# Performance work log

Hardware: AMD Instinct MI355X
Metric: run time of the kernel (lower is better)

Reference implementation:

```python
import jax, jax.numpy as jnp
import numpy as np

BL = 512  # block length (matches init bl)


def _conv1x1(w, b, x):
    # w: (out, in), b: (out,), x: (batch, in, L) -> (batch, out, L)
    return jnp.einsum('oi,bil->bol', w, x) + b[None, :, None]


def _window_mask(bl):
    # Faithful to torch loop: window_mask[:, :, i:i+bl] = 1 for i in range(bl)
    # -> all ones except the last column.
    wm = np.zeros((1, bl, bl + 2 * (bl // 2)), np.float32)
    for i in range(bl):
        wm[:, :, i:i + bl] = 1.0
    return jnp.asarray(wm)


def setup_inputs() -> dict:
    key = jax.random.key(0)
    ks = jax.random.split(key, 5)
    B, C, L = 1, 2048, 16384
    Cq = C // 2  # r1 = r2 = r3 = 2
    s_in = 1.0 / float(np.sqrt(C))
    s_mid = 1.0 / float(np.sqrt(Cq))
    return {
        'x1': jax.random.normal(ks[0], (B, C, L), jnp.float32),
        'x2': jnp.zeros((B, C, L), jnp.float32),
        'mask': jnp.ones((B, 1, L), jnp.float32),
        'wq': jax.random.normal(ks[1], (Cq, C), jnp.float32) * s_in,
        'bq': jnp.zeros((Cq,), jnp.float32),
        'wk': jax.random.normal(ks[2], (Cq, C), jnp.float32) * s_in,
        'bk': jnp.zeros((Cq,), jnp.float32),
        'wv': jax.random.normal(ks[3], (Cq, C), jnp.float32) * s_in,
        'bv': jnp.zeros((Cq,), jnp.float32),
        'wo': jax.random.normal(ks[4], (C, Cq), jnp.float32) * s_mid,
        'bo': jnp.zeros((C,), jnp.float32),
    }


def reference(x1, x2, mask, wq, bq, wk, bk, wv, bv, wo, bo):
    B, C, L = x1.shape  # B == 1 (asserted by sliding path)
    bl = BL
    nb = L // bl  # L % bl == 0 by construction
    half = bl // 2

    q = _conv1x1(wq, bq, x1)  # (1, c, L)
    k = _conv1x1(wk, bk, x1)
    v = _conv1x1(wv, bv, x1)  # encoder stage: value from x1 (x2 unused)
    c = q.shape[1]

    # query blocks: (nb, c, bl)
    qb = q.reshape(B, c, nb, bl).transpose(0, 2, 1, 3).reshape(nb, c, bl)

    # pad k/v/padding_mask with bl//2 zeros on both sides, then take overlapping
    # windows of width 2*bl per block.
    kp = jnp.pad(k, ((0, 0), (0, 0), (half, half)))[0]            # (c, L+bl)
    vp = jnp.pad(v, ((0, 0), (0, 0), (half, half)))[0]
    pm = jnp.pad(mask[:, 0:1, :], ((0, 0), (0, 0), (half, half)))[0]  # (1, L+bl)
    cols = np.arange(nb)[:, None] * bl + np.arange(2 * bl)[None, :]   # (nb, 2bl)
    kb = kp[:, cols].transpose(1, 0, 2)   # (nb, c, 2bl)
    vb = vp[:, cols].transpose(1, 0, 2)   # (nb, c, 2bl)
    pmb = pm[:, cols].transpose(1, 0, 2)  # (nb, 1, 2bl)

    final_mask = _window_mask(bl) * pmb   # (nb, bl, 2bl)

    # scalar dot attention with log-mask (as in AttentionHelper.scalar_dot_att)
    energy = jnp.einsum('ncl,ncm->nlm', qb, kb) / jnp.float32(np.sqrt(c))
    attn = jax.nn.softmax(energy + jnp.log(final_mask + 1e-9), axis=-1)
    attn = attn * final_mask
    out = jnp.einsum('ncm,nlm->ncl', vb, attn)  # (nb, c, bl)

    out = _conv1x1(wo, bo, jax.nn.relu(out))    # (nb, C, bl)
    out = out.reshape(B, nb, C, bl).transpose(0, 2, 1, 3).reshape(B, C, nb * bl)
    out = out[:, :, :L]
    return out * mask[:, 0:1, :]
```

## Files before the change

### kernel.cpp

```cpp
#include <hip/hip_runtime.h>
#include <hip/hip_bf16.h>

typedef __attribute__((ext_vector_type(4))) float f32x4;
typedef __attribute__((ext_vector_type(8))) __bf16 bf16x8;

#define DEVINL static __device__ __forceinline__

DEVINL unsigned short f2bf(float f) {
  union { float f; unsigned u; } x; x.f = f;
  return (unsigned short)((x.u + 0x7FFFu + ((x.u >> 16) & 1u)) >> 16);
}

DEVINL void gload16(const void* g, void* l) {
  __builtin_amdgcn_global_load_lds((const __attribute__((address_space(1))) void*)g,
                                   (__attribute__((address_space(3))) void*)l,
                                   16, 0, 0);
}

#define SBAR()  asm volatile("s_barrier" ::: "memory")
#define LGKM0() asm volatile("s_waitcnt lgkmcnt(0)" ::: "memory")
#define VM(n)   asm volatile("s_waitcnt vmcnt(" #n ")" ::: "memory")

__global__ __launch_bounds__(256) void transpose_x_k(const float* __restrict__ x,
                                                     unsigned short* __restrict__ xT) {
  __shared__ float tile[32][33];
  const int bx = blockIdx.x;
  const int by = blockIdx.y;
  const int tx = threadIdx.x;
  const int ty = threadIdx.y;
#pragma unroll
  for (int i = 0; i < 4; ++i) {
    int c = by * 32 + ty + i * 8;
    tile[ty + i * 8][tx] = x[(long)c * 16384 + bx * 32 + tx];
  }
  __syncthreads();
#pragma unroll
  for (int i = 0; i < 4; ++i) {
    int l = bx * 32 + ty + i * 8;
    xT[(long)l * 2048 + by * 32 + tx] = f2bf(tile[tx][ty + i * 8]);
  }
}

__global__ __launch_bounds__(256) void conv_w_k(const float* __restrict__ wq,
                                                const float* __restrict__ wk,
                                                const float* __restrict__ wv,
                                                const float* __restrict__ wo,
                                                unsigned short* __restrict__ Wqk,
                                                unsigned short* __restrict__ Wv,
                                                unsigned short* __restrict__ Wo) {
  long i = (long)blockIdx.x * 256 + threadIdx.x;
  if (i < 4194304) {
    float s = (i < 2097152) ? wq[i] : wk[i - 2097152];
    Wqk[i] = f2bf(s);
  } else if (i < 6291456) {
    Wv[i - 4194304] = f2bf(wv[i - 4194304]);
  } else {
    Wo[i - 6291456] = f2bf(wo[i - 6291456]);
  }
}

enum { EPI_QK = 0, EPI_V = 1, EPI_S = 2, EPI_PV = 3, EPI_OUT = 4 };

struct GArgs {
  const unsigned short* A;
  const unsigned short* Bt;
  void* C;
  const float* bias;
  const float* bias2;
  const float* mask;
  const unsigned short* guard;
  int aBatch, cBatch;
  int btRow0, btRow0Step, btRowLim;
  int btK0, btK0Step, btKLim;
};

template <int EPI, int LDA, int LDB, int LDC, int KK>
__global__ __launch_bounds__(512, 2) void gemm8_k(GArgs g) {
  constexpr int NK = KK >> 6;
  constexpr int NT = NK >> 1;
  __shared__ char lds[131072];

  const int t = threadIdx.x;
  const int l = t & 63;
  const int w = t >> 6;
  const int Nbase = blockIdx.x << 8;
  const int Mbase = blockIdx.y << 8;
  const int z = blockIdx.z;

  const int wr = w >> 2;
  const int wc = w & 3;
  const int fr = l & 15;
  const int fg = l >> 4;

  const unsigned short* Ab = g.A + (long)z * g.aBatch + (long)Mbase * LDA;
  const int bRowBase = g.btRow0 + z * g.btRow0Step + Nbase;
  const int bK0 = g.btK0 + z * g.btK0Step;

  const int rr = t >> 3;
  const int cb8s = t & 7;

  auto stage = [&](int bufSel, int unit, int kt) {
    const int k0 = (kt & (NK - 1)) << 6;
    const bool isA = (unit == 0) || (unit == 3);
#pragma unroll
    for (int gph = 0; gph < 2; ++gph) {
      int row;
      if (isA) row = (unit == 0 ? 0 : 64) + (gph << 7) + rr;
      else     row = (unit == 1 ? 0 : 32) + (gph << 7) + (rr & 31) + ((rr >> 5) << 6);
      const int cbL = cb8s ^ (row & 7);
      const int gk = k0 + (cbL << 3);
      char* lp = lds + (bufSel << 16) + (isA ? 0 : 32768) + row * 128 + (cb8s << 4);
      const char* gp;
      if (isA) {
        gp = (const char*)(Ab + (long)row * LDA + gk);
      } else {
        const int grow = bRowBase + row;
        const int gkk = bK0 + gk;
        if ((unsigned)grow < (unsigned)g.btRowLim && (unsigned)gkk < (unsigned)g.btKLim)
          gp = (const char*)(g.Bt + (long)grow * LDB + gkk);
        else
          gp = (const char*)g.guard + (l << 4);
      }
      gload16(gp, lp);
    }
  };

  const int arow = (wr << 7) + fr;
  const int brow = (wc << 6) + fr;

  auto ldA = [&](int i8, int kk, int bufSel) -> bf16x8 {
    const int row = arow + (i8 << 4);
    const int cb = ((kk << 2) | fg) ^ (row & 7);
    return *(const bf16x8*)(lds + (bufSel << 16) + row * 128 + (cb << 4));
  };
  auto ldB = [&](int j, int kk, int bufSel) -> bf16x8 {
    const int row = brow + (j << 4);
    const int cb = ((kk << 2) | fg) ^ (row & 7);
    return *(const bf16x8*)(lds + (bufSel << 16) + 32768 + row * 128 + (cb << 4));
  };

  f32x4 acc[8][4];
#pragma unroll
  for (int i = 0; i < 8; ++i)
#pragma unroll
    for (int j = 0; j < 4; ++j) acc[i][j] = f32x4{0.f, 0.f, 0.f, 0.f};

  stage(0, 0, 0); stage(0, 1, 0); stage(0, 2, 0); stage(0, 3, 0);
  stage(1, 0, 1); stage(1, 1, 1); stage(1, 2, 1);
  VM(6);
  SBAR();

  bf16x8 fa[4][2], fb[4][2];

#define MFMA_Q(QI, QJ)                                                        \
  __builtin_amdgcn_s_setprio(1);                                             \
  _Pragma("unroll") for (int i = 0; i < 4; ++i)                               \
  _Pragma("unroll") for (int j = 0; j < 2; ++j)                               \
  _Pragma("unroll") for (int kk = 0; kk < 2; ++kk)                            \
    acc[(QI)*4 + i][(QJ)*2 + j] = __builtin_amdgcn_mfma_f32_16x16x32_bf16(    \
        fa[i][kk], fb[(QJ)*2 + j][kk], acc[(QI)*4 + i][(QJ)*2 + j], 0, 0, 0); \
  __builtin_amdgcn_s_setprio(0);

#pragma unroll 1
  for (int it = 0; it < NT; ++it) {
    const int kt1 = 2 * it + 1;
    const int ktn0 = 2 * it + 2;
    const int ktn1 = 2 * it + 3;
#pragma unroll
    for (int i = 0; i < 4; ++i) { fa[i][0] = ldA(i, 0, 0); fa[i][1] = ldA(i, 1, 0); }
#pragma unroll
    for (int j = 0; j < 2; ++j) { fb[j][0] = ldB(j, 0, 0); fb[j][1] = ldB(j, 1, 0); }
    stage(1, 3, kt1);
    SBAR(); LGKM0();
    MFMA_Q(0, 0);
    SBAR();
#pragma unroll
    for (int j = 2; j < 4; ++j) { fb[j][0] = ldB(j, 0, 0); fb[j][1] = ldB(j, 1, 0); }
    stage(0, 0, ktn0);
    SBAR(); LGKM0();
    MFMA_Q(0, 1);
    SBAR();
#pragma unroll
    for (int i = 0; i < 4; ++i) { fa[i][0] = ldA(4 + i, 0, 0); fa[i][1] = ldA(4 + i, 1, 0); }
    stage(0, 1, ktn0);
    SBAR(); LGKM0();
    MFMA_Q(1, 0);
    SBAR();
    stage(0, 2, ktn0);
    SBAR(); LGKM0();
    MFMA_Q(1, 1);
    VM(6);
    SBAR();
#pragma unroll
    for (int i = 0; i < 4; ++i) { fa[i][0] = ldA(i, 0, 1); fa[i][1] = ldA(i, 1, 1); }
#pragma unroll
    for (int j = 0; j < 2; ++j) { fb[j][0] = ldB(j, 0, 1); fb[j][1] = ldB(j, 1, 1); }
    stage(0, 3, ktn0);
    SBAR(); LGKM0();
    MFMA_Q(0, 0);
    SBAR();
#pragma unroll
    for (int j = 2; j < 4; ++j) { fb[j][0] = ldB(j, 0, 1); fb[j][1] = ldB(j, 1, 1); }
    stage(1, 0, ktn1);
    SBAR(); LGKM0();
    MFMA_Q(0, 1);
    SBAR();
#pragma unroll
    for (int i = 0; i < 4; ++i) { fa[i][0] = ldA(4 + i, 0, 1); fa[i][1] = ldA(4 + i, 1, 1); }
    stage(1, 1, ktn1);
    SBAR(); LGKM0();
    MFMA_Q(1, 0);
    SBAR();
    stage(1, 2, ktn1);
    SBAR(); LGKM0();
    MFMA_Q(1, 1);
    VM(6);
    SBAR();
  }
  VM(0);
  SBAR();

#pragma unroll
  for (int ii = 0; ii < 8; ++ii)
#pragma unroll
    for (int j = 0; j < 4; ++j)
#pragma unroll
      for (int r = 0; r < 4; ++r) {
        const int row = Mbase + (wr << 7) + ii * 16 + fg * 4 + r;
        const int col = Nbase + (wc << 6) + j * 16 + fr;
        float val = acc[ii][j][r];
        const long off = (long)z * g.cBatch + (long)row * LDC + col;
        if (EPI == EPI_QK) {
          val = (col < 1024) ? (val + g.bias[col]) * 0.03125f
                             : (val + g.bias2[col - 1024]);
          ((unsigned short*)g.C)[off] = f2bf(val);
        } else if (EPI == EPI_V) {
          val += g.bias[row];
          ((unsigned short*)g.C)[off] = f2bf(val);
        } else if (EPI == EPI_S) {
          ((float*)g.C)[off] = val;
        } else if (EPI == EPI_PV) {
          val = fmaxf(val, 0.f);
          ((unsigned short*)g.C)[off] = f2bf(val);
        } else {
          val = (val + g.bias[row]) * g.mask[col];
          ((float*)g.C)[off] = val;
        }
      }
#undef MFMA_Q
}

__global__ __launch_bounds__(256) void softmax_k(const float* __restrict__ S,
                                                 const float* __restrict__ mask,
                                                 unsigned short* __restrict__ P) {
  const int row = blockIdx.x;
  const int n = row >> 9;
  const float* s = S + (long)row * 1024;
  unsigned short* p = P + (long)row * 1024;
  const int t = threadIdx.x;

  float logit[4], fm[4];
  float lmax = -3.0e38f;
#pragma unroll
  for (int i = 0; i < 4; ++i) {
    int m = i * 256 + t;
    int pos = (n << 9) + m - 256;
    float f = (((unsigned)pos < 16384u) && (m != 1023)) ? mask[pos] : 0.f;
    float lg = s[m] + logf(f + 1e-9f);
    fm[i] = f; logit[i] = lg;
    lmax = fmaxf(lmax, lg);
  }
#pragma unroll
  for (int o = 32; o; o >>= 1) lmax = fmaxf(lmax, __shfl_xor(lmax, o, 64));
  __shared__ float red[8];
  const int wv_ = t >> 6, ln = t & 63;
  if (ln == 0) red[wv_] = lmax;
  __syncthreads();
  const float gmax = fmaxf(fmaxf(red[0], red[1]), fmaxf(red[2], red[3]));

  float e[4], lsum = 0.f;
#pragma unroll
  for (int i = 0; i < 4; ++i) { e[i] = expf(logit[i] - gmax); lsum += e[i]; }
#pragma unroll
  for (int o = 32; o; o >>= 1) lsum += __shfl_xor(lsum, o, 64);
  __syncthreads();
  if (ln == 0) red[4 + wv_] = lsum;
  __syncthreads();
  const float inv = 1.f / ((red[4] + red[5]) + (red[6] + red[7]));
#pragma unroll
  for (int i = 0; i < 4; ++i) {
    int m = i * 256 + t;
    p[m] = f2bf(e[i] * inv * fm[i]);
  }
}

extern "C" void kernel_launch(void* const* d_in, const int* in_sizes, int n_in,
                              void* d_out, int out_size, void* d_ws, size_t ws_size,
                              hipStream_t stream) {
  const float* x1 = (const float*)d_in[0];
  const float* mask = (const float*)d_in[2];
  const float* wq = (const float*)d_in[3];
  const float* bq = (const float*)d_in[4];
  const float* wk = (const float*)d_in[5];
  const float* bk = (const float*)d_in[6];
  const float* wv = (const float*)d_in[7];
  const float* bv = (const float*)d_in[8];
  const float* wo = (const float*)d_in[9];
  const float* bo = (const float*)d_in[10];

  char* ws = (char*)d_ws;
  unsigned short* xT   = (unsigned short*)(ws);
  unsigned short* attT = xT;
  unsigned short* Wqk  = (unsigned short*)(ws + 67108864);
  unsigned short* Wv   = (unsigned short*)(ws + 75497472);
  unsigned short* Wo   = (unsigned short*)(ws + 79691776);
  unsigned short* qkT  = (unsigned short*)(ws + 83886080);
  unsigned short* vbuf = (unsigned short*)(ws + 150994944);
  float*          Sbuf = (float*)(ws + 184549376);
  unsigned short* P    = (unsigned short*)(ws + 251658240);
  unsigned short* guard= (unsigned short*)(ws + 285212672);

  hipMemsetAsync(guard, 0, 4096, stream);

  transpose_x_k<<<dim3(512, 64), dim3(32, 8), 0, stream>>>(x1, xT);
  conv_w_k<<<dim3(32768), dim3(256), 0, stream>>>(wq, wk, wv, wo, Wqk, Wv, Wo);

  const int BIG = 0x40000000;
  {
    GArgs a{};
    a.A = xT; a.Bt = Wqk; a.C = qkT;
    a.bias = bq; a.bias2 = bk; a.guard = guard;
    a.aBatch = 0; a.cBatch = 0;
    a.btRow0 = 0; a.btRow0Step = 0; a.btRowLim = BIG;
    a.btK0 = 0; a.btK0Step = 0; a.btKLim = BIG;
    gemm8_k<EPI_QK, 2048, 2048, 2048, 2048><<<dim3(8, 64, 1), 512, 0, stream>>>(a);
  }
  {
    GArgs a{};
    a.A = Wv; a.Bt = xT; a.C = vbuf;
    a.bias = bv; a.guard = guard;
    a.aBatch = 0; a.cBatch = 0;
    a.btRow0 = 0; a.btRow0Step = 0; a.btRowLim = BIG;
    a.btK0 = 0; a.btK0Step = 0; a.btKLim = BIG;
    gemm8_k<EPI_V, 2048, 2048, 16384, 2048><<<dim3(64, 4, 1), 512, 0, stream>>>(a);
  }
  {
    GArgs a{};
    a.A = qkT; a.Bt = qkT; a.C = Sbuf;
    a.guard = guard;
    a.aBatch = 512 * 2048; a.cBatch = 512 * 1024;
    a.btRow0 = -256; a.btRow0Step = 512; a.btRowLim = 16384;
    a.btK0 = 1024; a.btK0Step = 0; a.btKLim = BIG;
    gemm8_k<EPI_S, 2048, 2048, 1024, 1024><<<dim3(4, 2, 32), 512, 0, stream>>>(a);
  }
  softmax_k<<<dim3(16384), dim3(256), 0, stream>>>(Sbuf, mask, P);
  {
    GArgs a{};
    a.A = P; a.Bt = vbuf; a.C = attT;
    a.guard = guard;
    a.aBatch = 512 * 1024; a.cBatch = 512 * 1024;
    a.btRow0 = 0; a.btRow0Step = 0; a.btRowLim = BIG;
    a.btK0 = -256; a.btK0Step = 512; a.btKLim = 16384;
    gemm8_k<EPI_PV, 1024, 16384, 1024, 1024><<<dim3(4, 2, 32), 512, 0, stream>>>(a);
  }
  {
    GArgs a{};
    a.A = Wo; a.Bt = attT; a.C = d_out;
    a.bias = bo; a.mask = mask; a.guard = guard;
    a.aBatch = 0; a.cBatch = 0;
    a.btRow0 = 0; a.btRow0Step = 0; a.btRowLim = BIG;
    a.btK0 = 0; a.btK0Step = 0; a.btKLim = BIG;
    gemm8_k<EPI_OUT, 1024, 1024, 16384, 1024><<<dim3(64, 8, 1), 512, 0, stream>>>(a);
  }
  (void)in_sizes; (void)n_in; (void)out_size; (void)ws_size;
}
```

Before: 502.6 us.

## Software-pipeline LDS fragment reads with partial lgkmcnt waits and XCD-aware block remap

Rewrites the GEMM main loop so LDS fragment reads for the next quarter are issued before the current MFMA block. Full lgkmcnt(0) waits become partial waits and sched_barrier keeps the compiler from reordering. The A fragment register array doubles to hold all eight rows, and the prologue preloads the first fragments. Workgroup IDs are also remapped across the eight XCDs to improve L2 locality. This adds register pressure and fragile wait counts that could break correctness or occupancy.

```diff
diff --git a/kernel.cpp b/kernel.cpp
--- a/kernel.cpp
+++ b/kernel.cpp
@@ -17,9 +17,10 @@
                                    16, 0, 0);
 }
 
-#define SBAR()  asm volatile("s_barrier" ::: "memory")
-#define LGKM0() asm volatile("s_waitcnt lgkmcnt(0)" ::: "memory")
-#define VM(n)   asm volatile("s_waitcnt vmcnt(" #n ")" ::: "memory")
+#define SBAR()   asm volatile("s_barrier" ::: "memory")
+#define LGKM(n)  asm volatile("s_waitcnt lgkmcnt(" #n ")" ::: "memory")
+#define VM(n)    asm volatile("s_waitcnt vmcnt(" #n ")" ::: "memory")
+#define SCHED0() __builtin_amdgcn_sched_barrier(0)
 
 __global__ __launch_bounds__(256) void transpose_x_k(const float* __restrict__ x,
                                                      unsigned short* __restrict__ xT) {
@@ -83,9 +84,15 @@
   const int t = threadIdx.x;
   const int l = t & 63;
   const int w = t >> 6;
-  const int Nbase = blockIdx.x << 8;
-  const int Mbase = blockIdx.y << 8;
-  const int z = blockIdx.z;
+
+  const int gx = gridDim.x, gxy = gx * gridDim.y;
+  const int nwg = gxy * gridDim.z;
+  int lin = blockIdx.z * gxy + blockIdx.y * gx + blockIdx.x;
+  lin = (lin & 7) * (nwg >> 3) + (lin >> 3);
+  const int z = lin / gxy;
+  const int rres = lin - z * gxy;
+  const int Mbase = (rres / gx) << 8;
+  const int Nbase = (rres - (rres / gx) * gx) << 8;
 
   const int wr = w >> 2;
   const int wc = w & 3;
@@ -145,80 +152,67 @@
 #pragma unroll
     for (int j = 0; j < 4; ++j) acc[i][j] = f32x4{0.f, 0.f, 0.f, 0.f};
 
-  stage(0, 0, 0); stage(0, 1, 0); stage(0, 2, 0); stage(0, 3, 0);
-  stage(1, 0, 1); stage(1, 1, 1); stage(1, 2, 1);
-  VM(6);
-  SBAR();
-
-  bf16x8 fa[4][2], fb[4][2];
-
-#define MFMA_Q(QI, QJ)                                                        \
-  __builtin_amdgcn_s_setprio(1);                                             \
+  bf16x8 fa[8][2], fb[4][2];
+
+#define RD_FA03(b) _Pragma("unroll") for (int i = 0; i < 4; ++i) { fa[i][0] = ldA(i, 0, b); fa[i][1] = ldA(i, 1, b); }
+#define RD_FA47(b) _Pragma("unroll") for (int i = 4; i < 8; ++i) { fa[i][0] = ldA(i, 0, b); fa[i][1] = ldA(i, 1, b); }
+#define RD_FB01(b) _Pragma("unroll") for (int j = 0; j < 2; ++j) { fb[j][0] = ldB(j, 0, b); fb[j][1] = ldB(j, 1, b); }
+#define RD_FB23(b) _Pragma("unroll") for (int j = 2; j < 4; ++j) { fb[j][0] = ldB(j, 0, b); fb[j][1] = ldB(j, 1, b); }
+
+#define MQ(I0, J0)                                                            \
+  __builtin_amdgcn_s_setprio(1);                                              \
   _Pragma("unroll") for (int i = 0; i < 4; ++i)                               \
   _Pragma("unroll") for (int j = 0; j < 2; ++j)                               \
   _Pragma("unroll") for (int kk = 0; kk < 2; ++kk)                            \
-    acc[(QI)*4 + i][(QJ)*2 + j] = __builtin_amdgcn_mfma_f32_16x16x32_bf16(    \
-        fa[i][kk], fb[(QJ)*2 + j][kk], acc[(QI)*4 + i][(QJ)*2 + j], 0, 0, 0); \
+    acc[(I0) + i][(J0) + j] = __builtin_amdgcn_mfma_f32_16x16x32_bf16(        \
+        fa[(I0) + i][kk], fb[(J0) + j][kk], acc[(I0) + i][(J0) + j], 0, 0, 0);\
   __builtin_amdgcn_s_setprio(0);
+
+  stage(0, 0, 0); stage(0, 1, 0); stage(0, 2, 0); stage(0, 3, 0);
+  stage(1, 0, 1); stage(1, 1, 1); stage(1, 2, 1);
+  VM(8);
+  SBAR();
+  RD_FA03(0); RD_FB01(0);
 
 #pragma unroll 1
   for (int it = 0; it < NT; ++it) {
     const int kt1 = 2 * it + 1;
     const int ktn0 = 2 * it + 2;
     const int ktn1 = 2 * it + 3;
-#pragma unroll
-    for (int i = 0; i < 4; ++i) { fa[i][0] = ldA(i, 0, 0); fa[i][1] = ldA(i, 1, 0); }
-#pragma unroll
-    for (int j = 0; j < 2; ++j) { fb[j][0] = ldB(j, 0, 0); fb[j][1] = ldB(j, 1, 0); }
-    stage(1, 3, kt1);
-    SBAR(); LGKM0();
-    MFMA_Q(0, 0);
+    RD_FB23(0); stage(1, 3, kt1);
+    LGKM(4); SCHED0();
+    MQ(0, 0);
+    VM(8); SBAR();
+    RD_FA47(0); stage(0, 0, ktn0);
+    LGKM(8); SCHED0();
+    MQ(0, 2);
     SBAR();
-#pragma unroll
-    for (int j = 2; j < 4; ++j) { fb[j][0] = ldB(j, 0, 0); fb[j][1] = ldB(j, 1, 0); }
-    stage(0, 0, ktn0);
-    SBAR(); LGKM0();
-    MFMA_Q(0, 1);
+    stage(0, 1, ktn0);
+    LGKM(0); SCHED0();
+    MQ(4, 0);
+    VM(8); SBAR();
+    RD_FA03(1); RD_FB01(1); stage(0, 2, ktn0);
+    LGKM(12); SCHED0();
+    MQ(4, 2);
+    VM(8); SBAR();
+    RD_FB23(1); stage(0, 3, ktn0);
+    LGKM(4); SCHED0();
+    MQ(0, 0);
+    VM(8); SBAR();
+    RD_FA47(1); stage(1, 0, ktn1);
+    LGKM(8); SCHED0();
+    MQ(0, 2);
     SBAR();
-#pragma unroll
-    for (int i = 0; i < 4; ++i) { fa[i][0] = ldA(4 + i, 0, 0); fa[i][1] = ldA(4 + i, 1, 0); }
-    stage(0, 1, ktn0);
-    SBAR(); LGKM0();
-    MFMA_Q(1, 0);
-    SBAR();
-    stage(0, 2, ktn0);
-    SBAR(); LGKM0();
-    MFMA_Q(1, 1);
-    VM(6);
-    SBAR();
-#pragma unroll
-    for (int i = 0; i < 4; ++i) { fa[i][0] = ldA(i, 0, 1); fa[i][1] = ldA(i, 1, 1); }
-#pragma unroll
-    for (int j = 0; j < 2; ++j) { fb[j][0] = ldB(j, 0, 1); fb[j][1] = ldB(j, 1, 1); }
-    stage(0, 3, ktn0);
-    SBAR(); LGKM0();
-    MFMA_Q(0, 0);
-    SBAR();
-#pragma unroll
-    for (int j = 2; j < 4; ++j) { fb[j][0] = ldB(j, 0, 1); fb[j][1] = ldB(j, 1, 1); }
-    stage(1, 0, ktn1);
-    SBAR(); LGKM0();
-    MFMA_Q(0, 1);
-    SBAR();
-#pragma unroll
-    for (int i = 0; i < 4; ++i) { fa[i][0] = ldA(4 + i, 0, 1); fa[i][1] = ldA(4 + i, 1, 1); }
     stage(1, 1, ktn1);
-    SBAR(); LGKM0();
-    MFMA_Q(1, 0);
-    SBAR();
-    stage(1, 2, ktn1);
-    SBAR(); LGKM0();
-    MFMA_Q(1, 1);
-    VM(6);
-    SBAR();
-  }
-  VM(0);
-  SBAR();
+    LGKM(0); SCHED0();
+    MQ(4, 0);
+    VM(8); SBAR();
+    RD_FA03(0); RD_FB01(0); stage(1, 2, ktn1);
+    LGKM(12); SCHED0();
+    MQ(4, 2);
+    VM(8); SBAR();
+  }
+  VM(0); LGKM(0); SBAR();
 
 #pragma unroll
   for (int ii = 0; ii < 8; ++ii)
@@ -247,7 +241,11 @@
           ((float*)g.C)[off] = val;
         }
       }
-#undef MFMA_Q
+#undef MQ
+#undef RD_FA03
+#undef RD_FA47
+#undef RD_FB01
+#undef RD_FB23
 }
 
 __global__ __launch_bounds__(256) void softmax_k(const float* __restrict__ S,
```

Result: slower. 759.0 us (+51.0%).
